# Optimization experiments

Hardware: AMD Instinct MI355X
Metric: run time of the kernel (lower is better)

## Reference

```python
import jax, jax.numpy as jnp
import numpy as np

N = 100000          # nodes
E = 1_600_000       # edges (before self loops)
IN = 128            # in_channels
HID = 64            # hidden
HEADS = 4
EPS = 1e-5          # BatchNorm eps
NEG_SLOPE = 0.2     # GATConv leaky_relu slope


def setup_inputs() -> dict:
    key = jax.random.key(0)
    ks = jax.random.split(key, 16)
    he = lambda fan: (2.0 / fan) ** 0.5  # kaiming-normal scale
    d = {
        "x": jax.random.normal(ks[0], (N, IN), jnp.float32),
        "edge_index": jax.random.randint(ks[1], (2, E), 0, N, dtype=jnp.int64),
        "root_index": 0,
        "W1": jax.random.normal(ks[2], (IN, HEADS * HID), jnp.float32) * he(IN),
        "att_src1": jax.random.normal(ks[3], (HEADS, HID), jnp.float32) * 0.1,
        "att_dst1": jax.random.normal(ks[4], (HEADS, HID), jnp.float32) * 0.1,
        "b1": jnp.zeros((HEADS * HID,), jnp.float32),
        "W2": jax.random.normal(ks[5], (HEADS * HID, HID), jnp.float32) * he(HEADS * HID),
        "att_src2": jax.random.normal(ks[6], (1, HID), jnp.float32) * 0.1,
        "att_dst2": jax.random.normal(ks[7], (1, HID), jnp.float32) * 0.1,
        "b2": jnp.zeros((HID,), jnp.float32),
        "bn1_g": jnp.ones((HEADS * HID,), jnp.float32),
        "bn1_b": jnp.zeros((HEADS * HID,), jnp.float32),
        "bn1_m": jnp.zeros((HEADS * HID,), jnp.float32),
        "bn1_v": jnp.ones((HEADS * HID,), jnp.float32),
        "bn2_g": jnp.ones((HID,), jnp.float32),
        "bn2_b": jnp.zeros((HID,), jnp.float32),
        "bn2_m": jnp.zeros((HID,), jnp.float32),
        "bn2_v": jnp.ones((HID,), jnp.float32),
        "cg1_w": jax.random.normal(ks[8], (3 * HID, 64), jnp.float32) * he(3 * HID),
        "cg1_b": jnp.zeros((64,), jnp.float32),
        "cbn_g": jnp.ones((64,), jnp.float32),
        "cbn_b": jnp.zeros((64,), jnp.float32),
        "cbn_m": jnp.zeros((64,), jnp.float32),
        "cbn_v": jnp.ones((64,), jnp.float32),
        "cg2_w": jax.random.normal(ks[9], (64, 32), jnp.float32) * he(64),
        "cg2_b": jnp.zeros((32,), jnp.float32),
        "cg3_w": jax.random.normal(ks[10], (32, 1), jnp.float32) * he(32),
        "cg3_b": jnp.zeros((1,), jnp.float32),
    }
    return d


def _bn_eval(x, g, b, m, v):
    return (x - m) * jax.lax.rsqrt(v + EPS) * g + b


def _gat_conv(x, src, dst, W, att_src, att_dst, bias, heads, out_ch, concat):
    """PyG GATConv (eval mode, self loops already in src/dst)."""
    n = x.shape[0]
    h = (x @ W).reshape(n, heads, out_ch)                # [N,H,C]
    a_src = jnp.einsum('nhc,hc->nh', h, att_src)         # [N,H]
    a_dst = jnp.einsum('nhc,hc->nh', h, att_dst)
    e = jax.nn.leaky_relu(a_src[src] + a_dst[dst], NEG_SLOPE)   # [Etot,H]
    seg_max = jax.ops.segment_max(e, dst, num_segments=n)
    ex = jnp.exp(e - seg_max[dst])
    denom = jax.ops.segment_sum(ex, dst, num_segments=n)
    alpha = ex / (denom[dst] + 1e-16)                    # [Etot,H]
    msg = h[src] * alpha[:, :, None]                     # [Etot,H,C]
    out = jax.ops.segment_sum(msg, dst, num_segments=n)  # [N,H,C]
    if concat:
        return out.reshape(n, heads * out_ch) + bias
    return out.mean(axis=1) + bias


def reference(x, edge_index, root_index, W1, att_src1, att_dst1, b1,
              W2, att_src2, att_dst2, b2,
              bn1_g, bn1_b, bn1_m, bn1_v, bn2_g, bn2_b, bn2_m, bn2_v,
              cg1_w, cg1_b, cbn_g, cbn_b, cbn_m, cbn_v,
              cg2_w, cg2_b, cg3_w, cg3_b):
    n = x.shape[0]
    # add self loops (PyG GATConv default)
    loop = jnp.arange(n, dtype=edge_index.dtype)
    src = jnp.concatenate([edge_index[0], loop])
    dst = jnp.concatenate([edge_index[1], loop])

    h = _gat_conv(x, src, dst, W1, att_src1, att_dst1, b1, HEADS, HID, True)
    h = jax.nn.elu(_bn_eval(h, bn1_g, bn1_b, bn1_m, bn1_v))
    h = _gat_conv(h, src, dst, W2, att_src2, att_dst2, b2, 1, HID, False)
    node_emb = jax.nn.elu(_bn_eval(h, bn2_g, bn2_b, bn2_m, bn2_v))  # [N,HID]

    mean_emb = node_emb.mean(axis=0, keepdims=True)      # [1,HID]
    max_emb = node_emb.max(axis=0, keepdims=True)        # [1,HID]
    safe_root = min(root_index, n - 1)
    root_emb = node_emb[safe_root][None, :]              # single graph path
    g = jnp.concatenate([mean_emb, max_emb, root_emb], axis=-1)  # [1,3*HID]

    g = jax.nn.relu(_bn_eval(g @ cg1_w + cg1_b, cbn_g, cbn_b, cbn_m, cbn_v))
    g = jax.nn.relu(g @ cg2_w + cg2_b)
    logit = (g @ cg3_w + cg3_b).squeeze(-1)              # [1]
    return logit
```

## Files before the change

kernel.cpp:

```cpp
#include <hip/hip_runtime.h>

#define N_NODES 100000
#define N_EDGES 1600000
#define ETOT    1700000
#define IN_CH   128
#define C1      256
#define HID     64
#define BN_EPS  1e-5f
#define SLOPE   0.2f
#define NCHUNK  98
#define DEG_PH  8
#define DEG_PHN 12500
#define FILL_PH 12
#define FILL_PHN 8334

typedef __attribute__((ext_vector_type(8))) short s16x8;
typedef __attribute__((ext_vector_type(4))) float f32x4;
#define MFMA16(a, b, c) __builtin_amdgcn_mfma_f32_16x16x32_bf16(a, b, c, 0, 0, 0)

__device__ __forceinline__ float leaky(float x) { return fmaxf(x, SLOPE * x); }
__device__ __forceinline__ float elu_f(float x) { return x > 0.f ? x : __expf(x) - 1.f; }
__device__ __forceinline__ unsigned short f2bf(float f) {
  unsigned int b = __float_as_uint(f);
  return (unsigned short)((b + 0x7FFFu + ((b >> 16) & 1u)) >> 16);
}
__device__ __forceinline__ float bf2f(unsigned short u) {
  return __uint_as_float((unsigned int)u << 16);
}
__device__ __forceinline__ unsigned int encf(float f) {
  unsigned int b = __float_as_uint(f);
  return b ^ ((((int)b >> 31)) | 0x80000000u);
}
__device__ __forceinline__ float decf(unsigned int k) {
  unsigned int b = (k & 0x80000000u) ? (k ^ 0x80000000u) : ~k;
  return __uint_as_float(b);
}

__global__ void __launch_bounds__(256) k_prep_init(const float* __restrict__ W1, const float* __restrict__ W2,
                                                   unsigned short* __restrict__ W1T, unsigned short* __restrict__ W2T,
                                                   int* __restrict__ deg, float* __restrict__ psum,
                                                   unsigned int* __restrict__ pmaxenc) {
  int i = blockIdx.x * 256 + threadIdx.x;
  if (i < N_NODES) deg[i] = 1;
  if (i < IN_CH * C1) {
    int k = i >> 8, c = i & 255;
    W1T[c * IN_CH + k] = f2bf(W1[i]);
  }
  if (i < C1 * HID) {
    int k = i >> 6, c = i & 63;
    W2T[c * C1 + k] = f2bf(W2[i]);
  }
  if (i < 256 * 64) { psum[i] = 0.f; pmaxenc[i] = 0u; }
}

__global__ void __launch_bounds__(256) k_deg_ph(const int* __restrict__ edge, int* __restrict__ deg) {
  int bpp = (N_EDGES + 1023) >> 10;
  int ph = blockIdx.x / bpp;
  int lo = ph * DEG_PHN, hi = lo + DEG_PHN;
  int i0 = (blockIdx.x % bpp) * 1024 + threadIdx.x * 4;
  if (i0 >= N_EDGES) return;
  if (i0 + 3 < N_EDGES) {
    int4 dv = *(const int4*)(edge + N_EDGES + i0);
    if (dv.x >= lo && dv.x < hi) atomicAdd(&deg[dv.x], 1);
    if (dv.y >= lo && dv.y < hi) atomicAdd(&deg[dv.y], 1);
    if (dv.z >= lo && dv.z < hi) atomicAdd(&deg[dv.z], 1);
    if (dv.w >= lo && dv.w < hi) atomicAdd(&deg[dv.w], 1);
  } else {
    for (int j = 0; j < 4 && i0 + j < N_EDGES; j++) {
      int d = edge[N_EDGES + i0 + j];
      if (d >= lo && d < hi) atomicAdd(&deg[d], 1);
    }
  }
}

__global__ void __launch_bounds__(256) k_scan_part(const int* __restrict__ deg, int* __restrict__ part) {
  __shared__ int ls[256];
  int t = threadIdx.x;
  int base = blockIdx.x * 1024 + t * 4;
  int s = 0;
#pragma unroll
  for (int j = 0; j < 4; j++) if (base + j < N_NODES) s += deg[base + j];
  ls[t] = s;
  __syncthreads();
  for (int off = 128; off >= 1; off >>= 1) {
    if (t < off) ls[t] += ls[t + off];
    __syncthreads();
  }
  if (t == 0) part[blockIdx.x] = ls[0];
}

__global__ void k_scan_top(int* __restrict__ part, int* __restrict__ row_ptr) {
  if (threadIdx.x == 0 && blockIdx.x == 0) {
    int run = 0;
    for (int i = 0; i < NCHUNK; i++) { int t = part[i]; part[i] = run; run += t; }
    row_ptr[N_NODES] = run;
  }
}

__global__ void __launch_bounds__(256) k_scan_down(const int* __restrict__ deg, const int* __restrict__ part,
                                                   int* __restrict__ row_ptr, int* __restrict__ cursor) {
  __shared__ int ls[256];
  int t = threadIdx.x;
  int base = blockIdx.x * 1024 + t * 4;
  int v[4];
#pragma unroll
  for (int j = 0; j < 4; j++) v[j] = (base + j < N_NODES) ? deg[base + j] : 0;
  int tsum = v[0] + v[1] + v[2] + v[3];
  ls[t] = tsum;
  __syncthreads();
  for (int off = 1; off < 256; off <<= 1) {
    int add = (t >= off) ? ls[t - off] : 0;
    __syncthreads();
    ls[t] += add;
    __syncthreads();
  }
  int excl = ls[t] - tsum + part[blockIdx.x];
#pragma unroll
  for (int j = 0; j < 4; j++) {
    int idx = base + j;
    if (idx < N_NODES) { row_ptr[idx] = excl; cursor[idx] = excl; }
    excl += v[j];
  }
}

__global__ void __launch_bounds__(256) k_fill_ph(const int* __restrict__ edge, int* __restrict__ cursor,
                                                 const float* __restrict__ aS, const float* __restrict__ aD,
                                                 int* __restrict__ col, float* __restrict__ w1) {
  int bpp = (ETOT + 255) >> 8;
  int ph = blockIdx.x / bpp;
  int lo = ph * FILL_PHN, hi = lo + FILL_PHN;
  int i = (blockIdx.x % bpp) * 256 + threadIdx.x;
  if (i >= ETOT) return;
  int d = (i < N_EDGES) ? edge[N_EDGES + i] : (i - N_EDGES);
  if (d < lo || d >= hi) return;
  int s = (i < N_EDGES) ? edge[i] : d;
  int pos = atomicAdd(&cursor[d], 1);
  col[pos] = s;
  float4 as4 = *(const float4*)(aS + (size_t)s * 4);
  float4 ad4 = *(const float4*)(aD + (size_t)d * 4);
  float4 w;
  w.x = __expf(fminf(leaky(as4.x + ad4.x), 80.f));
  w.y = __expf(fminf(leaky(as4.y + ad4.y), 80.f));
  w.z = __expf(fminf(leaky(as4.z + ad4.z), 80.f));
  w.w = __expf(fminf(leaky(as4.w + ad4.w), 80.f));
  *(float4*)(w1 + (size_t)pos * 4) = w;
}

__global__ void __launch_bounds__(256) k_gemm1(const float* __restrict__ x, const unsigned short* __restrict__ W1T,
                                               const float* __restrict__ attS, const float* __restrict__ attD,
                                               unsigned short* __restrict__ h1b, float* __restrict__ aS,
                                               float* __restrict__ aD) {
  __shared__ unsigned short As[64][IN_CH + 8];
  int tid = threadIdx.x;
  int w = tid >> 6, lane = tid & 63;
  int l15 = lane & 15, l4 = lane >> 4;
  int row0 = blockIdx.x * 64;
#pragma unroll
  for (int it = 0; it < 8; it++) {
    int idx = tid + it * 256;
    int r = idx >> 5;
    int k4 = (idx & 31) * 4;
    int gr = row0 + r; if (gr >= N_NODES) gr = N_NODES - 1;
    float4 v = *(const float4*)(x + (size_t)gr * IN_CH + k4);
    ushort4 bvec;
    bvec.x = f2bf(v.x); bvec.y = f2bf(v.y); bvec.z = f2bf(v.z); bvec.w = f2bf(v.w);
    *(ushort4*)&As[r][k4] = bvec;
  }
  __syncthreads();
  f32x4 acc[4][4];
#pragma unroll
  for (int mf = 0; mf < 4; mf++)
#pragma unroll
    for (int cf = 0; cf < 4; cf++) acc[mf][cf] = (f32x4){0.f, 0.f, 0.f, 0.f};
#pragma unroll
  for (int ks = 0; ks < 4; ks++) {
    int koff = ks * 32 + l4 * 8;
    s16x8 a[4];
#pragma unroll
    for (int mf = 0; mf < 4; mf++) a[mf] = *(const s16x8*)&As[mf * 16 + l15][koff];
#pragma unroll
    for (int cf = 0; cf < 4; cf++) {
      s16x8 b = *(const s16x8*)(W1T + (size_t)(w * 64 + cf * 16 + l15) * IN_CH + koff);
#pragma unroll
      for (int mf = 0; mf < 4; mf++) acc[mf][cf] = MFMA16(a[mf], b, acc[mf][cf]);
    }
  }
  float as_c[4], ad_c[4];
#pragma unroll
  for (int cf = 0; cf < 4; cf++) {
    as_c[cf] = attS[w * HID + cf * 16 + l15];
    ad_c[cf] = attD[w * HID + cf * 16 + l15];
  }
#pragma unroll
  for (int mf = 0; mf < 4; mf++) {
#pragma unroll
    for (int reg = 0; reg < 4; reg++) {
      int gr = row0 + mf * 16 + l4 * 4 + reg;
      bool ok = gr < N_NODES;
      float s = 0.f, dd = 0.f;
#pragma unroll
      for (int cf = 0; cf < 4; cf++) {
        float v = acc[mf][cf][reg];
        if (ok) h1b[(size_t)gr * C1 + w * 64 + cf * 16 + l15] = f2bf(v);
        s += v * as_c[cf];
        dd += v * ad_c[cf];
      }
#pragma unroll
      for (int m = 1; m <= 8; m <<= 1) { s += __shfl_xor(s, m, 64); dd += __shfl_xor(dd, m, 64); }
      if (ok && l15 == 0) {
        aS[(size_t)gr * 4 + w] = s;
        aD[(size_t)gr * 4 + w] = dd;
      }
    }
  }
}

__global__ void __launch_bounds__(256) k_agg1(const int* __restrict__ row_ptr, const int* __restrict__ col,
                                              const float* __restrict__ w1,
                                              const unsigned short* __restrict__ h1b, const float* __restrict__ b1,
                                              const float* __restrict__ g1, const float* __restrict__ be1,
                                              const float* __restrict__ m1, const float* __restrict__ v1,
                                              unsigned short* __restrict__ hmb) {
  int wave = threadIdx.x >> 6;
  int lane = threadIdx.x & 63;
  int d = blockIdx.x * 4 + wave;
  if (d >= N_NODES) return;
  int head = lane >> 4;
  int s0 = row_ptr[d], s1 = row_ptr[d + 1];
  int s1m1 = s1 - 1;
  float denom = 0.f;
  float4 acc = {0.f, 0.f, 0.f, 0.f};
  int c0 = lane * 4;
  for (int base = s0; base < s1; base += 8) {
    int left = s1 - base;
    int idx = base + (lane & 7); if (idx > s1m1) idx = s1m1;
    int cv = col[idx];
    int sid[8];
#pragma unroll
    for (int j = 0; j < 8; j++) sid[j] = __builtin_amdgcn_readfirstlane(__shfl(cv, j));
    float wv[8];
#pragma unroll
    for (int j = 0; j < 8; j++) {
      int wi = base + j; if (wi > s1m1) wi = s1m1;
      float wl = w1[(size_t)wi * 4 + head];
      wv[j] = (j < left) ? wl : 0.f;
    }
    ushort4 h[8];
#pragma unroll
    for (int j = 0; j < 8; j++) h[j] = *(const ushort4*)(h1b + ((size_t)sid[j] << 8) + c0);
#pragma unroll
    for (int j = 0; j < 8; j++) {
      denom += wv[j];
      acc.x += wv[j] * bf2f(h[j].x);
      acc.y += wv[j] * bf2f(h[j].y);
      acc.z += wv[j] * bf2f(h[j].z);
      acc.w += wv[j] * bf2f(h[j].w);
    }
  }
  float inv = 1.f / (denom + 1e-16f);
  float4 bb = *(const float4*)(b1 + c0);
  float4 gg = *(const float4*)(g1 + c0);
  float4 be = *(const float4*)(be1 + c0);
  float4 mm = *(const float4*)(m1 + c0);
  float4 vv = *(const float4*)(v1 + c0);
  ushort4 o;
  o.x = f2bf(elu_f((acc.x * inv + bb.x - mm.x) * rsqrtf(vv.x + BN_EPS) * gg.x + be.x));
  o.y = f2bf(elu_f((acc.y * inv + bb.y - mm.y) * rsqrtf(vv.y + BN_EPS) * gg.y + be.y));
  o.z = f2bf(elu_f((acc.z * inv + bb.z - mm.z) * rsqrtf(vv.z + BN_EPS) * gg.z + be.z));
  o.w = f2bf(elu_f((acc.w * inv + bb.w - mm.w) * rsqrtf(vv.w + BN_EPS) * gg.w + be.w));
  *(ushort4*)(hmb + (size_t)d * C1 + c0) = o;
}

__global__ void __launch_bounds__(256) k_gemm2(const unsigned short* __restrict__ hmb, const unsigned short* __restrict__ W2T,
                                               const float* __restrict__ attS, const float* __restrict__ attD,
                                               unsigned short* __restrict__ h2b, float* __restrict__ aS,
                                               float* __restrict__ aD) {
  __shared__ unsigned short As[64][C1 + 8];
  int tid = threadIdx.x;
  int w = tid >> 6, lane = tid & 63;
  int l15 = lane & 15, l4 = lane >> 4;
  int row0 = blockIdx.x * 64;
#pragma unroll
  for (int it = 0; it < 8; it++) {
    int idx = tid + it * 256;
    int r = idx >> 5;
    int k8 = (idx & 31) * 8;
    int gr = row0 + r; if (gr >= N_NODES) gr = N_NODES - 1;
    *(uint4*)&As[r][k8] = *(const uint4*)(hmb + (size_t)gr * C1 + k8);
  }
  __syncthreads();
  f32x4 acc[4];
#pragma unroll
  for (int cf = 0; cf < 4; cf++) acc[cf] = (f32x4){0.f, 0.f, 0.f, 0.f};
#pragma unroll
  for (int ks = 0; ks < 8; ks++) {
    int koff = ks * 32 + l4 * 8;
    s16x8 a = *(const s16x8*)&As[w * 16 + l15][koff];
#pragma unroll
    for (int cf = 0; cf < 4; cf++) {
      s16x8 b = *(const s16x8*)(W2T + (size_t)(cf * 16 + l15) * C1 + koff);
      acc[cf] = MFMA16(a, b, acc[cf]);
    }
  }
  float as_c[4], ad_c[4];
#pragma unroll
  for (int cf = 0; cf < 4; cf++) {
    as_c[cf] = attS[cf * 16 + l15];
    ad_c[cf] = attD[cf * 16 + l15];
  }
#pragma unroll
  for (int reg = 0; reg < 4; reg++) {
    int gr = row0 + w * 16 + l4 * 4 + reg;
    bool ok = gr < N_NODES;
    float s = 0.f, dd = 0.f;
#pragma unroll
    for (int cf = 0; cf < 4; cf++) {
      float v = acc[cf][reg];
      if (ok) h2b[(size_t)gr * HID + cf * 16 + l15] = f2bf(v);
      s += v * as_c[cf];
      dd += v * ad_c[cf];
    }
#pragma unroll
    for (int m = 1; m <= 8; m <<= 1) { s += __shfl_xor(s, m, 64); dd += __shfl_xor(dd, m, 64); }
    if (ok && l15 == 0) { aS[gr] = s; aD[gr] = dd; }
  }
}

__global__ void __launch_bounds__(256) k_agg2(const int* __restrict__ row_ptr, const int* __restrict__ col,
                                              const float* __restrict__ aS, const float* __restrict__ aD,
                                              const unsigned short* __restrict__ h2b, const float* __restrict__ b2,
                                              const float* __restrict__ g2, const float* __restrict__ be2,
                                              const float* __restrict__ m2, const float* __restrict__ v2,
                                              const int* __restrict__ rootp, float* __restrict__ psum,
                                              unsigned int* __restrict__ pmaxenc, float* __restrict__ root_emb) {
  __shared__ float ss[4][64], sm[4][64];
  int wave = threadIdx.x >> 6;
  int lane = threadIdx.x & 63;
  int d = blockIdx.x * 4 + wave;
  float ad = aD[d];
  int s0 = row_ptr[d], s1 = row_ptr[d + 1];
  int s1m1 = s1 - 1;
  float denom = 0.f, acc = 0.f;
  for (int base = s0; base < s1; base += 8) {
    int left = s1 - base;
    int idx = base + (lane & 7); if (idx > s1m1) idx = s1m1;
    int cv = col[idx];
    int sid[8];
#pragma unroll
    for (int j = 0; j < 8; j++) sid[j] = __builtin_amdgcn_readfirstlane(__shfl(cv, j));
    float e[8];
#pragma unroll
    for (int j = 0; j < 8; j++) e[j] = aS[sid[j]];
    unsigned short h[8];
#pragma unroll
    for (int j = 0; j < 8; j++) h[j] = h2b[((size_t)sid[j] << 6) + lane];
    float wv[8];
#pragma unroll
    for (int j = 0; j < 8; j++) {
      float wl = __expf(fminf(leaky(e[j] + ad), 80.f));
      wv[j] = (j < left) ? wl : 0.f;
    }
#pragma unroll
    for (int j = 0; j < 8; j++) {
      denom += wv[j];
      acc += wv[j] * bf2f(h[j]);
    }
  }
  float o = acc / (denom + 1e-16f) + b2[lane];
  o = (o - m2[lane]) * rsqrtf(v2[lane] + BN_EPS) * g2[lane] + be2[lane];
  o = elu_f(o);
  ss[wave][lane] = o;
  sm[wave][lane] = o;
  int root0 = rootp[0];
  if (root0 > N_NODES - 1) root0 = N_NODES - 1;
  if (root0 < 0) root0 = 0;
  if (d == root0) root_emb[lane] = o;
  __syncthreads();
  if (threadIdx.x < 64) {
    int c = threadIdx.x;
    float s4 = ss[0][c] + ss[1][c] + ss[2][c] + ss[3][c];
    float m4 = fmaxf(fmaxf(sm[0][c], sm[1][c]), fmaxf(sm[2][c], sm[3][c]));
    int slot = (blockIdx.x & 255) * 64 + c;
    atomicAdd(&psum[slot], s4);
    atomicMax(&pmaxenc[slot], encf(m4));
  }
}

__global__ void __launch_bounds__(256) k_final(const float* __restrict__ psum, const unsigned int* __restrict__ pmaxenc,
                                               const float* __restrict__ root_emb,
                                               const float* __restrict__ cg1w, const float* __restrict__ cg1b,
                                               const float* __restrict__ cbng, const float* __restrict__ cbnb,
                                               const float* __restrict__ cbnm, const float* __restrict__ cbnv,
                                               const float* __restrict__ cg2w, const float* __restrict__ cg2b,
                                               const float* __restrict__ cg3w, const float* __restrict__ cg3b,
                                               float* __restrict__ out) {
  __shared__ float ss[4][64], sm[4][64];
  __shared__ float g[192], t1[64], t2[32];
  int t = threadIdx.x;
  int c = t & 63, q = t >> 6;
  float s = 0.f, m = -INFINITY;
  for (int b = q; b < 256; b += 4) {
    s += psum[b * 64 + c];
    m = fmaxf(m, decf(pmaxenc[b * 64 + c]));
  }
  ss[q][c] = s; sm[q][c] = m;
  __syncthreads();
  if (t < 64) {
    float tot = ss[0][t] + ss[1][t] + ss[2][t] + ss[3][t];
    float mx = fmaxf(fmaxf(sm[0][t], sm[1][t]), fmaxf(sm[2][t], sm[3][t]));
    g[t] = tot / (float)N_NODES;
    g[64 + t] = mx;
    g[128 + t] = root_emb[t];
  }
  __syncthreads();
  if (t < 64) {
    float o = cg1b[t];
    for (int i = 0; i < 192; i++) o += g[i] * cg1w[i * 64 + t];
    o = (o - cbnm[t]) * rsqrtf(cbnv[t] + BN_EPS) * cbng[t] + cbnb[t];
    t1[t] = o > 0.f ? o : 0.f;
  }
  __syncthreads();
  if (t < 32) {
    float o = cg2b[t];
    for (int i = 0; i < 64; i++) o += t1[i] * cg2w[i * 32 + t];
    t2[t] = o > 0.f ? o : 0.f;
  }
  __syncthreads();
  if (t == 0) {
    float o = cg3b[0];
    for (int i = 0; i < 32; i++) o += t2[i] * cg3w[i];
    out[0] = o;
  }
}

extern "C" void kernel_launch(void* const* d_in, const int* in_sizes, int n_in,
                              void* d_out, int out_size, void* d_ws, size_t ws_size,
                              hipStream_t stream) {
  const float* x     = (const float*)d_in[0];
  const int*   edge  = (const int*)d_in[1];
  const int*   root  = (const int*)d_in[2];
  const float* W1    = (const float*)d_in[3];
  const float* attS1 = (const float*)d_in[4];
  const float* attD1 = (const float*)d_in[5];
  const float* b1    = (const float*)d_in[6];
  const float* W2    = (const float*)d_in[7];
  const float* attS2 = (const float*)d_in[8];
  const float* attD2 = (const float*)d_in[9];
  const float* b2    = (const float*)d_in[10];
  const float* bn1g  = (const float*)d_in[11];
  const float* bn1b  = (const float*)d_in[12];
  const float* bn1m  = (const float*)d_in[13];
  const float* bn1v  = (const float*)d_in[14];
  const float* bn2g  = (const float*)d_in[15];
  const float* bn2b  = (const float*)d_in[16];
  const float* bn2m  = (const float*)d_in[17];
  const float* bn2v  = (const float*)d_in[18];
  const float* cg1w  = (const float*)d_in[19];
  const float* cg1b  = (const float*)d_in[20];
  const float* cbng  = (const float*)d_in[21];
  const float* cbnb  = (const float*)d_in[22];
  const float* cbnm  = (const float*)d_in[23];
  const float* cbnv  = (const float*)d_in[24];
  const float* cg2w  = (const float*)d_in[25];
  const float* cg2b  = (const float*)d_in[26];
  const float* cg3w  = (const float*)d_in[27];
  const float* cg3b  = (const float*)d_in[28];

  char* ws = (char*)d_ws;
  size_t off = 0;
  auto carve = [&](size_t bytes) { char* p = ws + off; off += (bytes + 255) & ~(size_t)255; return p; };
  unsigned short* h1b = (unsigned short*)carve((size_t)N_NODES * C1 * 2);
  unsigned short* hmb = (unsigned short*)carve((size_t)N_NODES * C1 * 2);
  float* w1      = (float*)carve((size_t)ETOT * 4 * 4);
  float* aS1     = (float*)carve((size_t)N_NODES * 4 * 4);
  float* aD1     = (float*)carve((size_t)N_NODES * 4 * 4);
  int*   deg     = (int*)  carve((size_t)N_NODES * 4);
  int*   row_ptr = (int*)  carve((size_t)(N_NODES + 1) * 4);
  int*   cursor  = (int*)  carve((size_t)N_NODES * 4);
  int*   col     = (int*)  carve((size_t)ETOT * 4);
  int*   part    = (int*)  carve(512);
  unsigned short* W1T = (unsigned short*)carve((size_t)IN_CH * C1 * 2);
  unsigned short* W2T = (unsigned short*)carve((size_t)C1 * HID * 2);
  float* psum    = (float*)carve(256 * 64 * 4);
  unsigned int* pmaxenc = (unsigned int*)carve(256 * 64 * 4);
  float* root_emb = (float*)carve(64 * 4);
  unsigned short* h2b = h1b;
  float* aS2  = (float*)(h1b + (size_t)N_NODES * HID);
  float* aD2  = aS2 + N_NODES;

  int bpp_deg  = (N_EDGES + 1023) >> 10;
  int bpp_fill = (ETOT + 255) >> 8;
  k_prep_init<<<(N_NODES + 255) / 256, 256, 0, stream>>>(W1, W2, W1T, W2T, deg, psum, pmaxenc);
  k_deg_ph<<<bpp_deg * DEG_PH, 256, 0, stream>>>(edge, deg);
  k_gemm1<<<(N_NODES + 63) / 64, 256, 0, stream>>>(x, W1T, attS1, attD1, h1b, aS1, aD1);
  k_scan_part<<<NCHUNK, 256, 0, stream>>>(deg, part);
  k_scan_top<<<1, 64, 0, stream>>>(part, row_ptr);
  k_scan_down<<<NCHUNK, 256, 0, stream>>>(deg, part, row_ptr, cursor);
  k_fill_ph<<<bpp_fill * FILL_PH, 256, 0, stream>>>(edge, cursor, aS1, aD1, col, w1);
  k_agg1<<<(N_NODES + 3) / 4, 256, 0, stream>>>(row_ptr, col, w1, h1b, b1, bn1g, bn1b, bn1m, bn1v, hmb);
  k_gemm2<<<(N_NODES + 63) / 64, 256, 0, stream>>>(hmb, W2T, attS2, attD2, h2b, aS2, aD2);
  k_agg2<<<N_NODES / 4, 256, 0, stream>>>(row_ptr, col, aS2, aD2, h2b, b2, bn2g, bn2b, bn2m, bn2v,
                                          root, psum, pmaxenc, root_emb);
  k_final<<<1, 256, 0, stream>>>(psum, pmaxenc, root_emb, cg1w, cg1b, cbng, cbnb, cbnm, cbnv,
                                 cg2w, cg2b, cg3w, cg3b, (float*)d_out);
}
```

Measured before the change: 478.0 us.

## Widen edge batches to 16 in aggregation, coalesce weights, drop phased degree count

```diff
diff --git a/kernel.cpp b/kernel.cpp
--- a/kernel.cpp
+++ b/kernel.cpp
@@ -9,8 +9,6 @@
 #define BN_EPS  1e-5f
 #define SLOPE   0.2f
 #define NCHUNK  98
-#define DEG_PH  8
-#define DEG_PHN 12500
 #define FILL_PH 12
 #define FILL_PHN 8334
 
@@ -53,24 +51,14 @@
   if (i < 256 * 64) { psum[i] = 0.f; pmaxenc[i] = 0u; }
 }
 
-__global__ void __launch_bounds__(256) k_deg_ph(const int* __restrict__ edge, int* __restrict__ deg) {
-  int bpp = (N_EDGES + 1023) >> 10;
-  int ph = blockIdx.x / bpp;
-  int lo = ph * DEG_PHN, hi = lo + DEG_PHN;
-  int i0 = (blockIdx.x % bpp) * 1024 + threadIdx.x * 4;
+__global__ void __launch_bounds__(256) k_deg(const int* __restrict__ edge, int* __restrict__ deg) {
+  int i0 = (blockIdx.x * 256 + threadIdx.x) * 4;
   if (i0 >= N_EDGES) return;
-  if (i0 + 3 < N_EDGES) {
-    int4 dv = *(const int4*)(edge + N_EDGES + i0);
-    if (dv.x >= lo && dv.x < hi) atomicAdd(&deg[dv.x], 1);
-    if (dv.y >= lo && dv.y < hi) atomicAdd(&deg[dv.y], 1);
-    if (dv.z >= lo && dv.z < hi) atomicAdd(&deg[dv.z], 1);
-    if (dv.w >= lo && dv.w < hi) atomicAdd(&deg[dv.w], 1);
-  } else {
-    for (int j = 0; j < 4 && i0 + j < N_EDGES; j++) {
-      int d = edge[N_EDGES + i0 + j];
-      if (d >= lo && d < hi) atomicAdd(&deg[d], 1);
-    }
-  }
+  int4 dv = *(const int4*)(edge + N_EDGES + i0);
+  atomicAdd(&deg[dv.x], 1);
+  atomicAdd(&deg[dv.y], 1);
+  atomicAdd(&deg[dv.z], 1);
+  atomicAdd(&deg[dv.w], 1);
 }
 
 __global__ void __launch_bounds__(256) k_scan_part(const int* __restrict__ deg, int* __restrict__ part) {
@@ -231,30 +219,28 @@
   float denom = 0.f;
   float4 acc = {0.f, 0.f, 0.f, 0.f};
   int c0 = lane * 4;
-  for (int base = s0; base < s1; base += 8) {
+  for (int base = s0; base < s1; base += 16) {
     int left = s1 - base;
-    int idx = base + (lane & 7); if (idx > s1m1) idx = s1m1;
+    int idx = base + (lane & 15); if (idx > s1m1) idx = s1m1;
     int cv = col[idx];
-    int sid[8];
-#pragma unroll
-    for (int j = 0; j < 8; j++) sid[j] = __builtin_amdgcn_readfirstlane(__shfl(cv, j));
-    float wv[8];
-#pragma unroll
-    for (int j = 0; j < 8; j++) {
-      int wi = base + j; if (wi > s1m1) wi = s1m1;
-      float wl = w1[(size_t)wi * 4 + head];
-      wv[j] = (j < left) ? wl : 0.f;
-    }
-    ushort4 h[8];
-#pragma unroll
-    for (int j = 0; j < 8; j++) h[j] = *(const ushort4*)(h1b + ((size_t)sid[j] << 8) + c0);
-#pragma unroll
-    for (int j = 0; j < 8; j++) {
-      denom += wv[j];
-      acc.x += wv[j] * bf2f(h[j].x);
-      acc.y += wv[j] * bf2f(h[j].y);
-      acc.z += wv[j] * bf2f(h[j].z);
-      acc.w += wv[j] * bf2f(h[j].w);
+    int widx = base * 4 + lane;
+    int wmax = s1 * 4 - 1; if (widx > wmax) widx = wmax;
+    float wflat = w1[widx];
+    int sid[16];
+#pragma unroll
+    for (int j = 0; j < 16; j++) sid[j] = __builtin_amdgcn_readfirstlane(__shfl(cv, j));
+    ushort4 h[16];
+#pragma unroll
+    for (int j = 0; j < 16; j++) h[j] = *(const ushort4*)(h1b + ((size_t)sid[j] << 8) + c0);
+#pragma unroll
+    for (int j = 0; j < 16; j++) {
+      float wl = __shfl(wflat, j * 4 + head);
+      float wv = (j < left) ? wl : 0.f;
+      denom += wv;
+      acc.x += wv * bf2f(h[j].x);
+      acc.y += wv * bf2f(h[j].y);
+      acc.z += wv * bf2f(h[j].z);
+      acc.w += wv * bf2f(h[j].w);
     }
   }
   float inv = 1.f / (denom + 1e-16f);
@@ -341,29 +327,25 @@
   int s0 = row_ptr[d], s1 = row_ptr[d + 1];
   int s1m1 = s1 - 1;
   float denom = 0.f, acc = 0.f;
-  for (int base = s0; base < s1; base += 8) {
+  for (int base = s0; base < s1; base += 16) {
     int left = s1 - base;
-    int idx = base + (lane & 7); if (idx > s1m1) idx = s1m1;
+    int idx = base + (lane & 15); if (idx > s1m1) idx = s1m1;
     int cv = col[idx];
-    int sid[8];
-#pragma unroll
-    for (int j = 0; j < 8; j++) sid[j] = __builtin_amdgcn_readfirstlane(__shfl(cv, j));
-    float e[8];
-#pragma unroll
-    for (int j = 0; j < 8; j++) e[j] = aS[sid[j]];
-    unsigned short h[8];
-#pragma unroll
-    for (int j = 0; j < 8; j++) h[j] = h2b[((size_t)sid[j] << 6) + lane];
-    float wv[8];
-#pragma unroll
-    for (int j = 0; j < 8; j++) {
+    int sid[16];
+#pragma unroll
+    for (int j = 0; j < 16; j++) sid[j] = __builtin_amdgcn_readfirstlane(__shfl(cv, j));
+    float e[16];
+#pragma unroll
+    for (int j = 0; j < 16; j++) e[j] = aS[sid[j]];
+    unsigned short h[16];
+#pragma unroll
+    for (int j = 0; j < 16; j++) h[j] = h2b[((size_t)sid[j] << 6) + lane];
+#pragma unroll
+    for (int j = 0; j < 16; j++) {
       float wl = __expf(fminf(leaky(e[j] + ad), 80.f));
-      wv[j] = (j < left) ? wl : 0.f;
-    }
-#pragma unroll
-    for (int j = 0; j < 8; j++) {
-      denom += wv[j];
-      acc += wv[j] * bf2f(h[j]);
+      float wv = (j < left) ? wl : 0.f;
+      denom += wv;
+      acc += wv * bf2f(h[j]);
     }
   }
   float o = acc / (denom + 1e-16f) + b2[lane];
@@ -488,10 +470,9 @@
   float* aS2  = (float*)(h1b + (size_t)N_NODES * HID);
   float* aD2  = aS2 + N_NODES;
 
-  int bpp_deg  = (N_EDGES + 1023) >> 10;
   int bpp_fill = (ETOT + 255) >> 8;
   k_prep_init<<<(N_NODES + 255) / 256, 256, 0, stream>>>(W1, W2, W1T, W2T, deg, psum, pmaxenc);
-  k_deg_ph<<<bpp_deg * DEG_PH, 256, 0, stream>>>(edge, deg);
+  k_deg<<<(N_EDGES / 4 + 255) / 256, 256, 0, stream>>>(edge, deg);
   k_gemm1<<<(N_NODES + 63) / 64, 256, 0, stream>>>(x, W1T, attS1, attD1, h1b, aS1, aD1);
   k_scan_part<<<NCHUNK, 256, 0, stream>>>(deg, part);
   k_scan_top<<<1, 64, 0, stream>>>(part, row_ptr);
```

Result: no change. 485.4 us (+1.6%).

## Split each node's layer-1 aggregation across four waves with LDS reduction

Applied to the files above, without the earlier changes.

```diff
diff --git a/kernel.cpp b/kernel.cpp
--- a/kernel.cpp
+++ b/kernel.cpp
@@ -221,19 +221,24 @@
                                               const float* __restrict__ g1, const float* __restrict__ be1,
                                               const float* __restrict__ m1, const float* __restrict__ v1,
                                               unsigned short* __restrict__ hmb) {
+  __shared__ float accs[4][64][4];
+  __shared__ float dens[4][64];
   int wave = threadIdx.x >> 6;
   int lane = threadIdx.x & 63;
-  int d = blockIdx.x * 4 + wave;
-  if (d >= N_NODES) return;
+  int d = blockIdx.x;
   int head = lane >> 4;
   int s0 = row_ptr[d], s1 = row_ptr[d + 1];
-  int s1m1 = s1 - 1;
+  int deg = s1 - s0;
+  int chunk = (deg + 3) >> 2;
+  int e0 = s0 + wave * chunk;
+  int e1 = e0 + chunk; if (e1 > s1) e1 = s1;
   float denom = 0.f;
   float4 acc = {0.f, 0.f, 0.f, 0.f};
   int c0 = lane * 4;
-  for (int base = s0; base < s1; base += 8) {
-    int left = s1 - base;
-    int idx = base + (lane & 7); if (idx > s1m1) idx = s1m1;
+  int e1m1 = e1 - 1;
+  for (int base = e0; base < e1; base += 8) {
+    int left = e1 - base;
+    int idx = base + (lane & 7); if (idx > e1m1) idx = e1m1;
     int cv = col[idx];
     int sid[8];
 #pragma unroll
@@ -241,7 +246,7 @@
     float wv[8];
 #pragma unroll
     for (int j = 0; j < 8; j++) {
-      int wi = base + j; if (wi > s1m1) wi = s1m1;
+      int wi = base + j; if (wi > e1m1) wi = e1m1;
       float wl = w1[(size_t)wi * 4 + head];
       wv[j] = (j < left) ? wl : 0.f;
     }
@@ -257,18 +262,29 @@
       acc.w += wv[j] * bf2f(h[j].w);
     }
   }
-  float inv = 1.f / (denom + 1e-16f);
-  float4 bb = *(const float4*)(b1 + c0);
-  float4 gg = *(const float4*)(g1 + c0);
-  float4 be = *(const float4*)(be1 + c0);
-  float4 mm = *(const float4*)(m1 + c0);
-  float4 vv = *(const float4*)(v1 + c0);
-  ushort4 o;
-  o.x = f2bf(elu_f((acc.x * inv + bb.x - mm.x) * rsqrtf(vv.x + BN_EPS) * gg.x + be.x));
-  o.y = f2bf(elu_f((acc.y * inv + bb.y - mm.y) * rsqrtf(vv.y + BN_EPS) * gg.y + be.y));
-  o.z = f2bf(elu_f((acc.z * inv + bb.z - mm.z) * rsqrtf(vv.z + BN_EPS) * gg.z + be.z));
-  o.w = f2bf(elu_f((acc.w * inv + bb.w - mm.w) * rsqrtf(vv.w + BN_EPS) * gg.w + be.w));
-  *(ushort4*)(hmb + (size_t)d * C1 + c0) = o;
+  *(float4*)&accs[wave][lane][0] = acc;
+  dens[wave][lane] = denom;
+  __syncthreads();
+  if (wave == 0) {
+#pragma unroll
+    for (int w2 = 1; w2 < 4; w2++) {
+      float4 a2 = *(const float4*)&accs[w2][lane][0];
+      acc.x += a2.x; acc.y += a2.y; acc.z += a2.z; acc.w += a2.w;
+      denom += dens[w2][lane];
+    }
+    float inv = 1.f / (denom + 1e-16f);
+    float4 bb = *(const float4*)(b1 + c0);
+    float4 gg = *(const float4*)(g1 + c0);
+    float4 be = *(const float4*)(be1 + c0);
+    float4 mm = *(const float4*)(m1 + c0);
+    float4 vv = *(const float4*)(v1 + c0);
+    ushort4 o;
+    o.x = f2bf(elu_f((acc.x * inv + bb.x - mm.x) * rsqrtf(vv.x + BN_EPS) * gg.x + be.x));
+    o.y = f2bf(elu_f((acc.y * inv + bb.y - mm.y) * rsqrtf(vv.y + BN_EPS) * gg.y + be.y));
+    o.z = f2bf(elu_f((acc.z * inv + bb.z - mm.z) * rsqrtf(vv.z + BN_EPS) * gg.z + be.z));
+    o.w = f2bf(elu_f((acc.w * inv + bb.w - mm.w) * rsqrtf(vv.w + BN_EPS) * gg.w + be.w));
+    *(ushort4*)(hmb + (size_t)d * C1 + c0) = o;
+  }
 }
 
 __global__ void __launch_bounds__(256) k_gemm2(const unsigned short* __restrict__ hmb, const unsigned short* __restrict__ W2T,
@@ -497,7 +513,7 @@
   k_scan_top<<<1, 64, 0, stream>>>(part, row_ptr);
   k_scan_down<<<NCHUNK, 256, 0, stream>>>(deg, part, row_ptr, cursor);
   k_fill_ph<<<bpp_fill * FILL_PH, 256, 0, stream>>>(edge, cursor, aS1, aD1, col, w1);
-  k_agg1<<<(N_NODES + 3) / 4, 256, 0, stream>>>(row_ptr, col, w1, h1b, b1, bn1g, bn1b, bn1m, bn1v, hmb);
+  k_agg1<<<N_NODES, 256, 0, stream>>>(row_ptr, col, w1, h1b, b1, bn1g, bn1b, bn1m, bn1v, hmb);
   k_gemm2<<<(N_NODES + 63) / 64, 256, 0, stream>>>(hmb, W2T, attS2, attD2, h2b, aS2, aD2);
   k_agg2<<<N_NODES / 4, 256, 0, stream>>>(row_ptr, col, aS2, aD2, h2b, b2, bn2g, bn2b, bn2m, bn2v,
                                           root, psum, pmaxenc, root_emb);
```

Result: slower. 504.5 us (+5.6%).
